# Kernel optimization log

Measured on AMD Instinct MI355X. Metric: run time of the kernel, lower is better.

The kernel has to match this reference:

```python
import jax, jax.numpy as jnp
import numpy as np

C_IN = 128
DIM = 2 * C_IN          # ELAN final channels = 2*in_channels = 256
WS = 8                  # window size
HEADS = 8
HEAD_DIM = DIM // HEADS
B, H, W = 4, 128, 128
LN_EPS = 1e-5


def setup_inputs() -> dict:
    key = jax.random.key(0)
    ks = jax.random.split(key, 20)
    mid = C_IN // 2  # middle_channels == block_channels == 64

    def p(k, shape, scale=0.05):
        return jax.random.normal(k, shape, jnp.float32) * scale

    return dict(
        x=jax.random.normal(ks[0], (B, C_IN, H, W), jnp.float32),
        # ELAN stem 1x1 convs: [main, short], each folded BN (scale, bias)
        w_stem=p(ks[1], (2, mid, C_IN, 1, 1)),
        s_stem=1.0 + p(ks[2], (2, mid)),
        b_stem=p(ks[3], (2, mid)),
        # 2 blocks x 2 convs of 3x3, mid->mid
        w_blk=p(ks[4], (4, mid, mid, 3, 3)),
        s_blk=1.0 + p(ks[5], (4, mid)),
        b_blk=p(ks[6], (4, mid)),
        # SwinV2 block params
        norm1_g=jnp.ones((DIM,), jnp.float32),
        norm1_b=jnp.zeros((DIM,), jnp.float32),
        qkv_w=p(ks[7], (3 * DIM, DIM)),
        qkv_b=p(ks[8], (3 * DIM,)).at[DIM:2 * DIM].set(0.0),  # V2 zeroes k bias
        proj_w=p(ks[9], (DIM, DIM)),
        proj_b=p(ks[10], (DIM,)),
        logit_scale=jnp.full((HEADS, 1, 1), float(np.log(10.0)), jnp.float32),
        cpb_w1=p(ks[11], (512, 2)),
        cpb_b1=p(ks[12], (512,)),
        cpb_w2=p(ks[13], (HEADS, 512)),
        norm2_g=jnp.ones((DIM,), jnp.float32),
        norm2_b=jnp.zeros((DIM,), jnp.float32),
        mlp_w1=p(ks[14], (DIM, DIM)),  # mlp_ratio=1.0
        mlp_b1=p(ks[15], (DIM,)),
        mlp_w2=p(ks[16], (DIM, DIM)),
        mlp_b2=p(ks[17], (DIM,)),
    )


def convbn(x, w, s, b, pad):
    # Conv(no bias) + eval-mode BN folded into per-channel scale/bias + SiLU
    y = jax.lax.conv_general_dilated(
        x, w, (1, 1), [(pad, pad), (pad, pad)],
        dimension_numbers=("NCHW", "OIHW", "NCHW"))
    y = y * s[None, :, None, None] + b[None, :, None, None]
    return jax.nn.silu(y)


def layernorm(x, g, b):
    m = jnp.mean(x, -1, keepdims=True)
    v = jnp.var(x, -1, keepdims=True)
    return (x - m) * jax.lax.rsqrt(v + LN_EPS) * g + b


def _rel_bias_consts():
    ws = WS
    ch = np.arange(-(ws - 1), ws, dtype=np.float32)
    table = np.stack(np.meshgrid(ch, ch, indexing="ij"), axis=-1)  # [2ws-1,2ws-1,2]
    table = table / (ws - 1) * 8.0
    table = np.sign(table) * np.log2(np.abs(table) + 1.0) / 3.0
    coords = np.stack(np.meshgrid(np.arange(ws), np.arange(ws), indexing="ij")).reshape(2, -1)
    rel = (coords[:, :, None] - coords[:, None, :]).transpose(1, 2, 0)  # [N,N,2]
    rel[..., 0] += ws - 1
    rel[..., 1] += ws - 1
    rel[..., 0] *= 2 * ws - 1
    idx = rel.sum(-1).reshape(-1)
    return jnp.asarray(table.reshape(-1, 2)), jnp.asarray(idx)


_TABLE, _IDX = _rel_bias_consts()


def elan_swin(x, w_stem, s_stem, b_stem, w_blk, s_blk, b_blk, norm1_g, norm1_b,
              qkv_w, qkv_b, proj_w, proj_b, logit_scale, cpb_w1, cpb_b1, cpb_w2,
              norm2_g, norm2_b, mlp_w1, mlp_b1, mlp_w2, mlp_b2):
    # ---- ELANBlock ----
    x_short = convbn(x, w_stem[1], s_stem[1], b_stem[1], 0)
    x_main = convbn(x, w_stem[0], s_stem[0], b_stem[0], 0)
    xb = x_main
    outs = []
    for i in range(2):
        xb = convbn(xb, w_blk[2 * i], s_blk[2 * i], b_blk[2 * i], 1)
        xb = convbn(xb, w_blk[2 * i + 1], s_blk[2 * i + 1], b_blk[2 * i + 1], 1)
        outs.append(xb)
    e = jnp.concatenate([outs[1], outs[0], x_main, x_short], axis=1)  # [B,DIM,H,W]
    e = e.transpose(0, 2, 3, 1)  # NHWC

    # ---- ShiftedWindowAttentionV2 (shift=0, H,W divisible by WS) ----
    Bn, Hh, Ww, Cc = e.shape
    nH, nW = Hh // WS, Ww // WS
    N = WS * WS
    xw = e.reshape(Bn, nH, WS, nW, WS, Cc).transpose(0, 1, 3, 2, 4, 5).reshape(-1, N, Cc)
    qkv = xw @ qkv_w.T + qkv_b
    qkv = qkv.reshape(-1, N, 3, HEADS, HEAD_DIM).transpose(2, 0, 3, 1, 4)
    q, k, v = qkv[0], qkv[1], qkv[2]  # [Bw, heads, N, d]
    qn = q / jnp.maximum(jnp.linalg.norm(q, axis=-1, keepdims=True), 1e-12)
    kn = k / jnp.maximum(jnp.linalg.norm(k, axis=-1, keepdims=True), 1e-12)
    attn = jnp.einsum("whnd,whmd->whnm", qn, kn)
    scale = jnp.exp(jnp.minimum(logit_scale, jnp.log(100.0)))  # [heads,1,1]
    attn = attn * scale[None]
    # continuous position bias MLP
    bias = jax.nn.relu(_TABLE @ cpb_w1.T + cpb_b1) @ cpb_w2.T  # [(2ws-1)^2, heads]
    bias = bias[_IDX].reshape(N, N, HEADS).transpose(2, 0, 1)
    bias = 16.0 * jax.nn.sigmoid(bias)
    attn = jax.nn.softmax(attn + bias[None], axis=-1)
    out = jnp.einsum("whnm,whmd->whnd", attn, v).transpose(0, 2, 1, 3).reshape(-1, N, Cc)
    out = out @ proj_w.T + proj_b
    out = out.reshape(Bn, nH, nW, WS, WS, Cc).transpose(0, 1, 3, 2, 4, 5).reshape(Bn, Hh, Ww, Cc)

    # ---- SwinTransformerBlockV2 (post-norm residuals) ----
    s = e + layernorm(out, norm1_g, norm1_b)
    h = s @ mlp_w1.T + mlp_b1
    h = jax.nn.gelu(h, approximate=False)
    h = h @ mlp_w2.T + mlp_b2
    s = s + layernorm(h, norm2_g, norm2_b)
    return s.transpose(0, 3, 1, 2)  # NCHW


def reference(x, w_stem, s_stem, b_stem, w_blk, s_blk, b_blk, norm1_g, norm1_b,
              qkv_w, qkv_b, proj_w, proj_b, logit_scale, cpb_w1, cpb_b1, cpb_w2,
              norm2_g, norm2_b, mlp_w1, mlp_b1, mlp_w2, mlp_b2):
    return elan_swin(x, w_stem, s_stem, b_stem, w_blk, s_blk, b_blk, norm1_g, norm1_b,
                     qkv_w, qkv_b, proj_w, proj_b, logit_scale, cpb_w1, cpb_b1, cpb_w2,
                     norm2_g, norm2_b, mlp_w1, mlp_b1, mlp_w2, mlp_b2)
```

## Files before the change

### kernel.cpp

```cpp
#include <hip/hip_runtime.h>
#include <hip/hip_bf16.h>
#include <math.h>


#define HW 16384
typedef unsigned int u32;
typedef unsigned short u16;
typedef __attribute__((ext_vector_type(8))) short short8;
typedef __attribute__((ext_vector_type(4))) float floatx4;

#define MEMBAR() asm volatile("" ::: "memory")

__device__ __forceinline__ float silu_f(float y) { return y / (1.f + expf(-y)); }
__device__ __forceinline__ float bflo(u32 u) { return __uint_as_float(u << 16); }
__device__ __forceinline__ float bfhi(u32 u) { return __uint_as_float(u & 0xffff0000u); }
__device__ __forceinline__ float bf2f(u16 v) { return __uint_as_float((u32)v << 16); }
__device__ __forceinline__ u16 f2bf(float x) {
  u32 u = __float_as_uint(x);
  u += 0x7fffu + ((u >> 16) & 1u);
  return (u16)(u >> 16);
}
__device__ __forceinline__ u32 pack2(float a, float b) {
  return (u32)f2bf(a) | ((u32)f2bf(b) << 16);
}
__device__ __forceinline__ short8 mk8(u32 a, u32 b, u32 c, u32 d) {
  union { u32 u[4]; short8 s; } t;
  t.u[0] = a; t.u[1] = b; t.u[2] = c; t.u[3] = d;
  return t.s;
}
__device__ __forceinline__ u32 shfl_sel(u32 va, u32 vb, int s, bool sel) {
  u32 x = (u32)__shfl((int)va, s);
  u32 y = (u32)__shfl((int)vb, s);
  return sel ? y : x;
}

#define GLDS16(gp, lp)                                           \
  __builtin_amdgcn_global_load_lds(                              \
      (const __attribute__((address_space(1))) void*)(gp),       \
      (__attribute__((address_space(3))) void*)(lp), 16, 0, 0)

__global__ __launch_bounds__(256) void repack_kernel(
    const float* __restrict__ w_blk, const float* __restrict__ s_blk,
    const float* __restrict__ w_stem, const float* __restrict__ s_stem,
    u16* __restrict__ wtc, u16* __restrict__ wts) {
  int idx = blockIdx.x * 256 + threadIdx.x;
  if (idx < 147456) {
    int c = idx & 63;
    int rest = idx >> 6;
    int oc = rest & 63;
    int ct = rest >> 6;
    int conv = ct / 9, t = ct % 9;
    float w = w_blk[((size_t)(conv * 64 + oc) * 64 + c) * 9 + t];
    wtc[idx] = f2bf(w * s_blk[conv * 64 + oc]);
  } else if (idx < 147456 + 16384) {
    int j = idx - 147456;
    int c = j & 127, oc = j >> 7;
    float w = w_stem[(size_t)oc * 128 + c];
    wts[j] = f2bf(w * s_stem[oc]);
  }
}

__global__ __launch_bounds__(256) void castw_kernel(
    const float* __restrict__ in, u16* __restrict__ outp, int n) {
  int i = blockIdx.x * 256 + threadIdx.x;
  if (i < n) outp[i] = f2bf(in[i]);
}

__global__ __launch_bounds__(512) void cpb_mlp_kernel(
    const float* __restrict__ w1, const float* __restrict__ b1,
    const float* __restrict__ w2, float* __restrict__ pre) {
  __shared__ float hb[512];
  int t = blockIdx.x, j = threadIdx.x;
  int i = t / 15, jj = t % 15;
  float c0 = (float)(i - 7) * (8.f / 7.f);
  float c1 = (float)(jj - 7) * (8.f / 7.f);
  float s0 = (c0 > 0.f) ? 1.f : ((c0 < 0.f) ? -1.f : 0.f);
  float s1 = (c1 > 0.f) ? 1.f : ((c1 < 0.f) ? -1.f : 0.f);
  float t0 = s0 * log2f(fabsf(c0) + 1.f) * (1.f / 3.f);
  float t1 = s1 * log2f(fabsf(c1) + 1.f) * (1.f / 3.f);
  float h = t0 * w1[j * 2] + t1 * w1[j * 2 + 1] + b1[j];
  hb[j] = fmaxf(h, 0.f);
  __syncthreads();
  if (j < 8) {
    float s = 0.f;
    for (int k = 0; k < 512; ++k) s += hb[k] * w2[j * 512 + k];
    pre[t * 8 + j] = s;
  }
}

__global__ __launch_bounds__(256) void cpb_expand_kernel(
    const float* __restrict__ pre, float* __restrict__ bias_t) {
  int idx = blockIdx.x * 256 + threadIdx.x;
  int m = idx >> 6, n = idx & 63;
  int di = (n >> 3) - (m >> 3) + 7;
  int dj = (n & 7) - (m & 7) + 7;
  int ti = di * 15 + dj;
#pragma unroll
  for (int h = 0; h < 8; ++h) {
    float v = pre[ti * 8 + h];
    bias_t[h * 4096 + idx] = 16.f / (1.f + expf(-v));
  }
}

__global__ __launch_bounds__(256) void transpose_in_kernel(
    const float* __restrict__ x, u16* __restrict__ xt) {
  __shared__ float tl[64][65];
  int bid = blockIdx.x;
  int b = bid >> 9;
  int r = bid & 511;
  int cs = r >> 8, hws = r & 255;
  int c0 = cs << 6, hw0 = hws << 6;
  int tid = threadIdx.x;
  for (int e = tid; e < 4096; e += 256) {
    int c = e >> 6, p = e & 63;
    tl[c][p] = x[(size_t)(b * 128 + c0 + c) * HW + hw0 + p];
  }
  __syncthreads();
  for (int e = tid; e < 4096; e += 256) {
    int p = e >> 6, c = e & 63;
    xt[(size_t)(b * HW + hw0 + p) * 128 + c0 + c] = f2bf(tl[c][p]);
  }
}

__global__ __launch_bounds__(256, 4) void gemm_bf16_kernel(
    const u16* __restrict__ A, const u16* __restrict__ W,
    const float* __restrict__ bias, u16* __restrict__ C, int K, int ldc,
    int act) {
  __shared__ u16 As[128 * 64];
  __shared__ u16 Ws[64 * 64];
  int tid = threadIdx.x;
  int wv = tid >> 6, lane = tid & 63;
  int m0 = blockIdx.y * 128, n0 = blockIdx.x * 64;
  floatx4 zz = {0.f, 0.f, 0.f, 0.f};
  floatx4 acc[2][4];
#pragma unroll
  for (int i = 0; i < 2; ++i)
#pragma unroll
    for (int j = 0; j < 4; ++j) acc[i][j] = zz;
  int lr = lane >> 3, ls = lane & 7;
  for (int k0 = 0; k0 < K; k0 += 64) {
#pragma unroll
    for (int i = 0; i < 4; ++i) {
      int ci = wv * 4 + i;
      int r = ci * 8 + lr;
      int cc = ls ^ (r & 7);
      GLDS16(A + (size_t)(m0 + r) * K + k0 + cc * 8, As + ci * 512);
    }
#pragma unroll
    for (int i = 0; i < 2; ++i) {
      int ci = wv * 2 + i;
      int r = ci * 8 + lr;
      int cc = ls ^ (r & 7);
      GLDS16(W + (size_t)(n0 + r) * K + k0 + cc * 8, Ws + ci * 512);
    }
    __syncthreads();
#pragma unroll
    for (int kk = 0; kk < 2; ++kk) {
      int g = kk * 4 + (lane >> 4);
      short8 a0, a1, b0, b1, b2, b3;
      {
        int row = wv * 32 + (lane & 15);
        a0 = *(const short8*)&As[row * 64 + (g ^ (row & 7)) * 8];
        int row2 = row + 16;
        a1 = *(const short8*)&As[row2 * 64 + (g ^ (row2 & 7)) * 8];
      }
      {
        int col = lane & 15;
        b0 = *(const short8*)&Ws[col * 64 + (g ^ (col & 7)) * 8];
        int c1 = col + 16;
        b1 = *(const short8*)&Ws[c1 * 64 + (g ^ (c1 & 7)) * 8];
        int c2 = col + 32;
        b2 = *(const short8*)&Ws[c2 * 64 + (g ^ (c2 & 7)) * 8];
        int c3 = col + 48;
        b3 = *(const short8*)&Ws[c3 * 64 + (g ^ (c3 & 7)) * 8];
      }
      acc[0][0] = __builtin_amdgcn_mfma_f32_16x16x32_bf16(a0, b0, acc[0][0], 0, 0, 0);
      acc[0][1] = __builtin_amdgcn_mfma_f32_16x16x32_bf16(a0, b1, acc[0][1], 0, 0, 0);
      acc[0][2] = __builtin_amdgcn_mfma_f32_16x16x32_bf16(a0, b2, acc[0][2], 0, 0, 0);
      acc[0][3] = __builtin_amdgcn_mfma_f32_16x16x32_bf16(a0, b3, acc[0][3], 0, 0, 0);
      acc[1][0] = __builtin_amdgcn_mfma_f32_16x16x32_bf16(a1, b0, acc[1][0], 0, 0, 0);
      acc[1][1] = __builtin_amdgcn_mfma_f32_16x16x32_bf16(a1, b1, acc[1][1], 0, 0, 0);
      acc[1][2] = __builtin_amdgcn_mfma_f32_16x16x32_bf16(a1, b2, acc[1][2], 0, 0, 0);
      acc[1][3] = __builtin_amdgcn_mfma_f32_16x16x32_bf16(a1, b3, acc[1][3], 0, 0, 0);
    }
    __syncthreads();
  }
  int rbase = wv * 32 + ((lane >> 4) << 2);
  int cb = lane & 15;
#pragma unroll
  for (int mi = 0; mi < 2; ++mi) {
#pragma unroll
    for (int nj = 0; nj < 4; ++nj) {
      int col = n0 + nj * 16 + cb;
      float bv = bias[col];
#pragma unroll
      for (int r = 0; r < 4; ++r) {
        int row = m0 + rbase + mi * 16 + r;
        float v = acc[mi][nj][r] + bv;
        if (act == 1) v = 0.5f * v * (1.f + erff(v * 0.70710678118654752f));
        else if (act == 2) v = silu_f(v);
        C[(size_t)row * ldc + col] = f2bf(v);
      }
    }
  }
}

__global__ __launch_bounds__(256) void conv3x3_mfma_kernel(
    const u16* __restrict__ in, int istr, u16* __restrict__ outp, int ostr,
    const u16* __restrict__ wt, const float* __restrict__ bias) {
  __shared__ u16 tile[6400];
  int tid = threadIdx.x;
  int wv = tid >> 6, lane = tid & 63;
  int bx = blockIdx.x, by = blockIdx.y, b = blockIdx.z;
  int h0 = by * 8, w0 = bx * 8;
#pragma unroll
  for (int rr = 0; rr < 4; ++rr) {
    int slot = rr * 256 + tid;
    int p = slot >> 3, ch = slot & 7;
    if (p < 100) {
      int hr = p / 10, hc = p % 10;
      int gh = h0 + hr - 1, gw = w0 + hc - 1;
      bool ok = (gh >= 0) && (gh < 128) && (gw >= 0) && (gw < 128);
      uint4 v = {0u, 0u, 0u, 0u};
      if (ok) {
        size_t pix = (size_t)((b * 128 + gh) * 128 + gw);
        v = *(const uint4*)(in + pix * istr + ch * 8);
      }
      *(uint4*)(tile + p * 64 + ((ch ^ (p & 7)) << 3)) = v;
    }
  }
  __syncthreads();
  int pl = lane & 15;
  int g = lane >> 4;
  int prow = 2 * wv + (pl >> 3), pcol = pl & 7;
  floatx4 zz = {0.f, 0.f, 0.f, 0.f};
  floatx4 acc[4] = {zz, zz, zz, zz};
#pragma unroll
  for (int t = 0; t < 9; ++t) {
    int dy = t / 3, dx = t % 3;
    int hp = (prow + dy) * 10 + (pcol + dx);
    short8 bf0 = *(const short8*)&tile[hp * 64 + (((0 * 4 + g) ^ (hp & 7)) << 3)];
    short8 bf1 = *(const short8*)&tile[hp * 64 + (((1 * 4 + g) ^ (hp & 7)) << 3)];
    const u16* wtap = wt + t * 4096;
#pragma unroll
    for (int nf = 0; nf < 4; ++nf) {
      short8 a0 = *(const short8*)&wtap[(nf * 16 + pl) * 64 + g * 8];
      short8 a1 = *(const short8*)&wtap[(nf * 16 + pl) * 64 + 32 + g * 8];
      acc[nf] = __builtin_amdgcn_mfma_f32_16x16x32_bf16(a0, bf0, acc[nf], 0, 0, 0);
      acc[nf] = __builtin_amdgcn_mfma_f32_16x16x32_bf16(a1, bf1, acc[nf], 0, 0, 0);
    }
  }
  size_t pix = (size_t)((b * 128 + h0 + prow) * 128 + w0 + pcol);
#pragma unroll
  for (int nf = 0; nf < 4; ++nf) {
    float o0 = silu_f(acc[nf][0] + bias[nf * 16 + g * 4 + 0]);
    float o1 = silu_f(acc[nf][1] + bias[nf * 16 + g * 4 + 1]);
    float o2 = silu_f(acc[nf][2] + bias[nf * 16 + g * 4 + 2]);
    float o3 = silu_f(acc[nf][3] + bias[nf * 16 + g * 4 + 3]);
    uint2 w2;
    w2.x = pack2(o0, o1);
    w2.y = pack2(o2, o3);
    *(uint2*)(outp + pix * ostr + nf * 16 + g * 4) = w2;
  }
}

__device__ __forceinline__ void qkv_mm(const u16* Elds, const u16* qwb,
                                       int moff, int h, int lc, int lg,
                                       floatx4 acc[4][2]) {
  floatx4 zz = {0.f, 0.f, 0.f, 0.f};
#pragma unroll
  for (int mf = 0; mf < 4; ++mf) {
    acc[mf][0] = zz;
    acc[mf][1] = zz;
  }
#pragma unroll
  for (int ks = 0; ks < 8; ++ks) {
    int ch = ks >> 1, g = ((ks & 1) << 2) + lg;
    short8 af[4];
#pragma unroll
    for (int mf = 0; mf < 4; ++mf) {
      int tk = mf * 16 + lc;
      af[mf] = *(const short8*)&Elds[(ch * 64 + tk) * 64 + ((g ^ (tk & 7)) << 3)];
    }
#pragma unroll
    for (int nf = 0; nf < 2; ++nf) {
      short8 bf = *(const short8*)(qwb +
          (size_t)(moff + h * 32 + nf * 16 + lc) * 256 + ks * 32 + lg * 8);
#pragma unroll
      for (int mf = 0; mf < 4; ++mf)
        acc[mf][nf] =
            __builtin_amdgcn_mfma_f32_16x16x32_bf16(af[mf], bf, acc[mf][nf], 0, 0, 0);
    }
  }
}

__global__ __launch_bounds__(512, 4) void attn_fused_kernel(
    const u16* __restrict__ ebf, const u16* __restrict__ qwb,
    const float* __restrict__ qkv_b, const float* __restrict__ logit_scale,
    const float* __restrict__ bias_t, u16* __restrict__ ao) {
  __shared__ __align__(16) char lds[73728];
  int tid = threadIdx.x;
  int w = tid >> 6, l = tid & 63;
  int wid = blockIdx.x;
  int h = __builtin_amdgcn_readfirstlane(w);
  u16* Elds = (u16*)lds;
  char* Sc = lds + 32768 + w * 5120;
  char* Ol = Sc;

  int b = wid >> 8, wh = (wid >> 4) & 15, ww = wid & 15;
  int pixbase = (b << 14) + wh * 1024 + ww * 8;
  {
    int lr = l >> 3, ls = l & 7;
    int ch = w >> 1;
#pragma unroll
    for (int j = 0; j < 4; ++j) {
      int jj = ((w & 1) << 2) + j;
      int pix = pixbase + jj * 128 + lr;
      GLDS16(ebf + (size_t)pix * 256 + ch * 64 + ((ls ^ lr) << 3),
             Elds + (ch * 8 + jj) * 512);
    }
  }
  __syncthreads();

  int lc = l & 15, lg = l >> 4;
  float scale = __expf(fminf(logit_scale[h], 4.6051701860f));
  floatx4 macc[4][2];
  short8 kf[4], qf[4];

  qkv_mm(Elds, qwb, 256, h, lc, lg, macc);
#pragma unroll
  for (int mf = 0; mf < 4; ++mf)
#pragma unroll
    for (int r = 0; r < 4; ++r) {
      float v0 = macc[mf][0][r], v1 = macc[mf][1][r];
      float ss = v0 * v0 + v1 * v1;
      ss += __shfl_xor(ss, 1);
      ss += __shfl_xor(ss, 2);
      ss += __shfl_xor(ss, 4);
      ss += __shfl_xor(ss, 8);
      float rk = 1.f / fmaxf(sqrtf(ss), 1e-12f);
      int tk = mf * 16 + (lg << 2) + r;
      *(u16*)(Sc + tk * 80 + lc * 2) = f2bf(v0 * rk);
      *(u16*)(Sc + tk * 80 + (16 + lc) * 2) = f2bf(v1 * rk);
    }
  MEMBAR();
#pragma unroll
  for (int i = 0; i < 4; ++i)
    kf[i] = *(const short8*)(Sc + (i * 16 + lc) * 80 + (lg << 4));
  MEMBAR();

  qkv_mm(Elds, qwb, 0, h, lc, lg, macc);
  {
    float qb0 = qkv_b[h * 32 + lc], qb1 = qkv_b[h * 32 + 16 + lc];
#pragma unroll
    for (int mf = 0; mf < 4; ++mf)
#pragma unroll
      for (int r = 0; r < 4; ++r) {
        float v0 = macc[mf][0][r] + qb0, v1 = macc[mf][1][r] + qb1;
        float ss = v0 * v0 + v1 * v1;
        ss += __shfl_xor(ss, 1);
        ss += __shfl_xor(ss, 2);
        ss += __shfl_xor(ss, 4);
        ss += __shfl_xor(ss, 8);
        float rq = scale / fmaxf(sqrtf(ss), 1e-12f);
        int tk = mf * 16 + (lg << 2) + r;
        *(u16*)(Sc + tk * 80 + lc * 2) = f2bf(v0 * rq);
        *(u16*)(Sc + tk * 80 + (16 + lc) * 2) = f2bf(v1 * rq);
      }
    MEMBAR();
#pragma unroll
    for (int i = 0; i < 4; ++i)
      qf[i] = *(const short8*)(Sc + (i * 16 + lc) * 80 + (lg << 4));
    MEMBAR();
  }

  u32 v01[4][2], v23[4][2];
  qkv_mm(Elds, qwb, 512, h, lc, lg, macc);
  {
    float vb0 = qkv_b[512 + h * 32 + lc], vb1 = qkv_b[512 + h * 32 + 16 + lc];
#pragma unroll
    for (int mf = 0; mf < 4; ++mf) {
      v01[mf][0] = pack2(macc[mf][0][0] + vb0, macc[mf][0][1] + vb0);
      v23[mf][0] = pack2(macc[mf][0][2] + vb0, macc[mf][0][3] + vb0);
      v01[mf][1] = pack2(macc[mf][1][0] + vb1, macc[mf][1][1] + vb1);
      v23[mf][1] = pack2(macc[mf][1][2] + vb1, macc[mf][1][3] + vb1);
    }
  }

  floatx4 zz = {0.f, 0.f, 0.f, 0.f};
  floatx4 S[4][4];
#pragma unroll
  for (int mi = 0; mi < 4; ++mi)
#pragma unroll
    for (int ni = 0; ni < 4; ++ni)
      S[mi][ni] = __builtin_amdgcn_mfma_f32_16x16x32_bf16(kf[mi], qf[ni], zz, 0, 0, 0);

  const float* bh = bias_t + h * 4096;
  float den[4] = {0.f, 0.f, 0.f, 0.f};
#pragma unroll
  for (int mi = 0; mi < 4; ++mi) {
    int mb = mi * 16 + (lg << 2);
#pragma unroll
    for (int ni = 0; ni < 4; ++ni) {
      int nn = ni * 16 + lc;
#pragma unroll
      for (int r = 0; r < 4; ++r) {
        float e = __expf(S[mi][ni][r] + bh[(mb + r) * 64 + nn]);
        S[mi][ni][r] = e;
        den[ni] += e;
      }
    }
  }
#pragma unroll
  for (int ni = 0; ni < 4; ++ni) {
    den[ni] += __shfl_xor(den[ni], 16);
    den[ni] += __shfl_xor(den[ni], 32);
    den[ni] = 1.f / den[ni];
  }
  u32 p01[4][4], p23[4][4];
#pragma unroll
  for (int mi = 0; mi < 4; ++mi)
#pragma unroll
    for (int ni = 0; ni < 4; ++ni) {
      p01[mi][ni] = pack2(S[mi][ni][0] * den[ni], S[mi][ni][1] * den[ni]);
      p23[mi][ni] = pack2(S[mi][ni][2] * den[ni], S[mi][ni][3] * den[ni]);
    }

  int s1 = ((lg & 1) << 5) + lc;
  int s2 = s1 + 16;
  bool hi = lg >= 2;
  short8 vf[2][2];
#pragma unroll
  for (int ks = 0; ks < 2; ++ks)
#pragma unroll
    for (int db = 0; db < 2; ++db) {
      u32 w0 = shfl_sel(v01[ks * 2][db], v01[ks * 2 + 1][db], s1, hi);
      u32 w1 = shfl_sel(v23[ks * 2][db], v23[ks * 2 + 1][db], s1, hi);
      u32 w2 = shfl_sel(v01[ks * 2][db], v01[ks * 2 + 1][db], s2, hi);
      u32 w3 = shfl_sel(v23[ks * 2][db], v23[ks * 2 + 1][db], s2, hi);
      vf[ks][db] = mk8(w0, w1, w2, w3);
    }
  floatx4 O[4][2];
#pragma unroll
  for (int nb = 0; nb < 4; ++nb) {
    u32 a0 = shfl_sel(p01[0][nb], p01[1][nb], s1, hi);
    u32 a1 = shfl_sel(p23[0][nb], p23[1][nb], s1, hi);
    u32 a2 = shfl_sel(p01[0][nb], p01[1][nb], s2, hi);
    u32 a3 = shfl_sel(p23[0][nb], p23[1][nb], s2, hi);
    short8 pf0 = mk8(a0, a1, a2, a3);
    u32 b0 = shfl_sel(p01[2][nb], p01[3][nb], s1, hi);
    u32 b1 = shfl_sel(p23[2][nb], p23[3][nb], s1, hi);
    u32 b2 = shfl_sel(p01[2][nb], p01[3][nb], s2, hi);
    u32 b3 = shfl_sel(p23[2][nb], p23[3][nb], s2, hi);
    short8 pf1 = mk8(b0, b1, b2, b3);
    floatx4 o0 = __builtin_amdgcn_mfma_f32_16x16x32_bf16(pf0, vf[0][0], zz, 0, 0, 0);
    o0 = __builtin_amdgcn_mfma_f32_16x16x32_bf16(pf1, vf[1][0], o0, 0, 0, 0);
    floatx4 o1 = __builtin_amdgcn_mfma_f32_16x16x32_bf16(pf0, vf[0][1], zz, 0, 0, 0);
    o1 = __builtin_amdgcn_mfma_f32_16x16x32_bf16(pf1, vf[1][1], o1, 0, 0, 0);
    O[nb][0] = o0;
    O[nb][1] = o1;
  }

#pragma unroll
  for (int nb = 0; nb < 4; ++nb)
#pragma unroll
    for (int r = 0; r < 4; ++r) {
      int n = nb * 16 + (lg << 2) + r;
      *(u16*)(Ol + n * 72 + lc * 2) = f2bf(O[nb][0][r]);
      *(u16*)(Ol + n * 72 + (16 + lc) * 2) = f2bf(O[nb][1][r]);
    }
  MEMBAR();
  u32 ov[16];
#pragma unroll
  for (int j = 0; j < 16; ++j) ov[j] = *(const u32*)(Ol + l * 72 + j * 4);
  uint4* op = (uint4*)(ao + (size_t)(wid * 64 + l) * 256 + h * 32);
#pragma unroll
  for (int q4 = 0; q4 < 4; ++q4) {
    uint4 v;
    v.x = ov[q4 * 4 + 0];
    v.y = ov[q4 * 4 + 1];
    v.z = ov[q4 * 4 + 2];
    v.w = ov[q4 * 4 + 3];
    op[q4] = v;
  }
}

__global__ __launch_bounds__(256) void ln1v_kernel(
    const u16* __restrict__ pin, const u16* __restrict__ ebf,
    u16* __restrict__ sbf, const float* __restrict__ g,
    const float* __restrict__ bb) {
  int tid = threadIdx.x;
  int bid = blockIdx.x;
  int b = bid >> 8, hw0 = (bid & 255) << 6;
  int i = tid >> 2, qq = tid & 3;
  int hw = hw0 + i;
  int him = hw >> 7, wim = hw & 127;
  int wid = b * 256 + (him >> 3) * 16 + (wim >> 3);
  int t = wid * 64 + (him & 7) * 8 + (wim & 7);
  size_t pbase = (size_t)t * 256 + qq * 64;
  size_t ebase = ((size_t)(b * HW + hw)) * 256 + qq * 64;
  float v[64];
  float s1 = 0.f, s2 = 0.f;
#pragma unroll
  for (int j = 0; j < 8; ++j) {
    uint4 u = *(const uint4*)(pin + pbase + j * 8);
    u32 ua[4] = {u.x, u.y, u.z, u.w};
#pragma unroll
    for (int k = 0; k < 4; ++k) {
      float a = bflo(ua[k]), c = bfhi(ua[k]);
      v[j * 8 + 2 * k] = a;
      v[j * 8 + 2 * k + 1] = c;
      s1 += a + c;
      s2 += a * a + c * c;
    }
  }
  s1 += __shfl_xor(s1, 1);
  s1 += __shfl_xor(s1, 2);
  s2 += __shfl_xor(s2, 1);
  s2 += __shfl_xor(s2, 2);
  float mean = s1 * (1.f / 256.f);
  float var = s2 * (1.f / 256.f) - mean * mean;
  float rs = rsqrtf(var + 1e-5f);
#pragma unroll
  for (int j = 0; j < 8; ++j) {
    uint4 u = *(const uint4*)(ebf + ebase + j * 8);
    u32 ua[4] = {u.x, u.y, u.z, u.w};
    uint4 o;
    u32 ow[4];
#pragma unroll
    for (int k = 0; k < 4; ++k) {
      int c = qq * 64 + j * 8 + 2 * k;
      float o0 = bflo(ua[k]) + (v[j * 8 + 2 * k] - mean) * rs * g[c] + bb[c];
      float o1 = bfhi(ua[k]) + (v[j * 8 + 2 * k + 1] - mean) * rs * g[c + 1] + bb[c + 1];
      ow[k] = pack2(o0, o1);
    }
    o.x = ow[0]; o.y = ow[1]; o.z = ow[2]; o.w = ow[3];
    *(uint4*)(sbf + ebase + j * 8) = o;
  }
}

__global__ __launch_bounds__(256) void ln2t_kernel(
    const u16* __restrict__ h2, const u16* __restrict__ sbf,
    const float* __restrict__ g, const float* __restrict__ bb,
    float* __restrict__ outp) {
  __shared__ float tile[64][257];
  int tid = threadIdx.x;
  int bid = blockIdx.x;
  int b = bid >> 8, hw0 = (bid & 255) << 6;
  int i = tid >> 2, qq = tid & 3;
  size_t base = ((size_t)(b * HW + hw0 + i)) * 256 + qq * 64;
  float v[64];
  float s1 = 0.f, s2 = 0.f;
#pragma unroll
  for (int j = 0; j < 8; ++j) {
    uint4 u = *(const uint4*)(h2 + base + j * 8);
    u32 ua[4] = {u.x, u.y, u.z, u.w};
#pragma unroll
    for (int k = 0; k < 4; ++k) {
      float a = bflo(ua[k]), c = bfhi(ua[k]);
      v[j * 8 + 2 * k] = a;
      v[j * 8 + 2 * k + 1] = c;
      s1 += a + c;
      s2 += a * a + c * c;
    }
  }
  s1 += __shfl_xor(s1, 1);
  s1 += __shfl_xor(s1, 2);
  s2 += __shfl_xor(s2, 1);
  s2 += __shfl_xor(s2, 2);
  float mean = s1 * (1.f / 256.f);
  float var = s2 * (1.f / 256.f) - mean * mean;
  float rs = rsqrtf(var + 1e-5f);
#pragma unroll
  for (int j = 0; j < 8; ++j) {
    uint4 u = *(const uint4*)(sbf + base + j * 8);
    u32 ua[4] = {u.x, u.y, u.z, u.w};
#pragma unroll
    for (int k = 0; k < 4; ++k) {
      int c = qq * 64 + j * 8 + 2 * k;
      tile[i][c] = bflo(ua[k]) + (v[j * 8 + 2 * k] - mean) * rs * g[c] + bb[c];
      tile[i][c + 1] = bfhi(ua[k]) + (v[j * 8 + 2 * k + 1] - mean) * rs * g[c + 1] + bb[c + 1];
    }
  }
  __syncthreads();
  int pl = tid & 63, cq = tid >> 6;
#pragma unroll 8
  for (int cc = 0; cc < 64; ++cc) {
    int c = cq * 64 + cc;
    outp[((size_t)(b * 256 + c)) * HW + hw0 + pl] = tile[pl][c];
  }
}

extern "C" void kernel_launch(void* const* d_in, const int* in_sizes, int n_in,
                              void* d_out, int out_size, void* d_ws, size_t ws_size,
                              hipStream_t stream) {
  const float* x        = (const float*)d_in[0];
  const float* w_stem   = (const float*)d_in[1];
  const float* s_stem   = (const float*)d_in[2];
  const float* b_stem   = (const float*)d_in[3];
  const float* w_blk    = (const float*)d_in[4];
  const float* s_blk    = (const float*)d_in[5];
  const float* b_blk    = (const float*)d_in[6];
  const float* norm1_g  = (const float*)d_in[7];
  const float* norm1_b  = (const float*)d_in[8];
  const float* qkv_w    = (const float*)d_in[9];
  const float* qkv_b    = (const float*)d_in[10];
  const float* proj_w   = (const float*)d_in[11];
  const float* proj_b   = (const float*)d_in[12];
  const float* logit_sc = (const float*)d_in[13];
  const float* cpb_w1   = (const float*)d_in[14];
  const float* cpb_b1   = (const float*)d_in[15];
  const float* cpb_w2   = (const float*)d_in[16];
  const float* norm2_g  = (const float*)d_in[17];
  const float* norm2_b  = (const float*)d_in[18];
  const float* mlp_w1   = (const float*)d_in[19];
  const float* mlp_b1   = (const float*)d_in[20];
  const float* mlp_w2   = (const float*)d_in[21];
  const float* mlp_b2   = (const float*)d_in[22];
  float* out = (float*)d_out;
  float* ws = (float*)d_ws;
  (void)in_sizes; (void)n_in; (void)out_size; (void)ws_size;

  float* R0 = ws;
  float* R1 = ws + 16777216;
  float* R2 = ws + 33554432;
  float* TAIL = ws + 50331648;
  u16* WTC  = (u16*)TAIL;
  u16* WTS  = (u16*)(TAIL + 73728);
  u16* QWB  = (u16*)(TAIL + 81920);
  u16* PWB  = (u16*)(TAIL + 180224);
  u16* M1WB = (u16*)(TAIL + 212992);
  u16* M2WB = (u16*)(TAIL + 245760);
  float* BPRE = TAIL + 278528;
  float* BFT  = TAIL + 280576;

  u16* XT  = (u16*)R2;
  u16* EBF = (u16*)(R2 + 8388608);
  u16* T1  = (u16*)R1;
  u16* T2  = (u16*)(R1 + 2097152);
  u16* AO  = (u16*)R0;
  u16* P   = (u16*)(R0 + 8388608);
  u16* SBF = (u16*)R0;
  u16* Hb  = (u16*)R2;
  u16* H2  = (u16*)(R0 + 8388608);

  repack_kernel<<<640, 256, 0, stream>>>(w_blk, s_blk, w_stem, s_stem, WTC, WTS);
  castw_kernel<<<768, 256, 0, stream>>>(qkv_w, QWB, 196608);
  castw_kernel<<<256, 256, 0, stream>>>(proj_w, PWB, 65536);
  castw_kernel<<<256, 256, 0, stream>>>(mlp_w1, M1WB, 65536);
  castw_kernel<<<256, 256, 0, stream>>>(mlp_w2, M2WB, 65536);
  cpb_mlp_kernel<<<225, 512, 0, stream>>>(cpb_w1, cpb_b1, cpb_w2, BPRE);
  cpb_expand_kernel<<<16, 256, 0, stream>>>(BPRE, BFT);

  transpose_in_kernel<<<2048, 256, 0, stream>>>(x, XT);
  dim3 gs(2, 512);
  gemm_bf16_kernel<<<gs, 256, 0, stream>>>(XT, WTS, b_stem, EBF + 128, 128, 256, 2);

  dim3 cgrid(16, 16, 4);
  conv3x3_mfma_kernel<<<cgrid, 256, 0, stream>>>(EBF + 128, 256, T1, 64, WTC, b_blk);
  conv3x3_mfma_kernel<<<cgrid, 256, 0, stream>>>(T1, 64, EBF + 64, 256, WTC + 9 * 4096, b_blk + 64);
  conv3x3_mfma_kernel<<<cgrid, 256, 0, stream>>>(EBF + 64, 256, T2, 64, WTC + 18 * 4096, b_blk + 128);
  conv3x3_mfma_kernel<<<cgrid, 256, 0, stream>>>(T2, 64, EBF, 256, WTC + 27 * 4096, b_blk + 192);

  attn_fused_kernel<<<1024, 512, 0, stream>>>(EBF, QWB, qkv_b, logit_sc, BFT, AO);

  dim3 g4(4, 512);
  gemm_bf16_kernel<<<g4, 256, 0, stream>>>(AO, PWB, proj_b, P, 256, 256, 0);
  ln1v_kernel<<<1024, 256, 0, stream>>>(P, EBF, SBF, norm1_g, norm1_b);
  gemm_bf16_kernel<<<g4, 256, 0, stream>>>(SBF, M1WB, mlp_b1, Hb, 256, 256, 1);
  gemm_bf16_kernel<<<g4, 256, 0, stream>>>(Hb, M2WB, mlp_b2, H2, 256, 256, 0);
  ln2t_kernel<<<1024, 256, 0, stream>>>(H2, SBF, norm2_g, norm2_b, out);
}
```

Measured before the change: 421.3 us.

## Fuse MLP second GEMM with LayerNorm2 and merge weight-cast kernels

Replaces the final mlp_w2 GEMM plus separate ln2t kernel with one kernel that computes a full 64x256 output tile, stages it in LDS, applies LayerNorm and the residual, and writes NCHW output directly. This removes the H2 intermediate round trip through global memory and one launch. It also merges the repack and four weight-cast kernels into a single prep kernel to cut launch overhead. The trade-off is that the fused kernel writes the output with strided per-element stores across channels instead of the old LDS-transposed coalesced stores, and it keeps 16 accumulators per wave.

```diff
diff --git a/kernel.cpp b/kernel.cpp
--- a/kernel.cpp
+++ b/kernel.cpp
@@ -39,10 +39,13 @@
       (const __attribute__((address_space(1))) void*)(gp),       \
       (__attribute__((address_space(3))) void*)(lp), 16, 0, 0)
 
-__global__ __launch_bounds__(256) void repack_kernel(
+__global__ __launch_bounds__(256) void prep_kernel(
     const float* __restrict__ w_blk, const float* __restrict__ s_blk,
     const float* __restrict__ w_stem, const float* __restrict__ s_stem,
-    u16* __restrict__ wtc, u16* __restrict__ wts) {
+    const float* __restrict__ qkv_w, const float* __restrict__ proj_w,
+    const float* __restrict__ mlp_w1, const float* __restrict__ mlp_w2,
+    u16* __restrict__ wtc, u16* __restrict__ wts, u16* __restrict__ qwb,
+    u16* __restrict__ pwb, u16* __restrict__ m1wb, u16* __restrict__ m2wb) {
   int idx = blockIdx.x * 256 + threadIdx.x;
   if (idx < 147456) {
     int c = idx & 63;
@@ -52,18 +55,23 @@
     int conv = ct / 9, t = ct % 9;
     float w = w_blk[((size_t)(conv * 64 + oc) * 64 + c) * 9 + t];
     wtc[idx] = f2bf(w * s_blk[conv * 64 + oc]);
-  } else if (idx < 147456 + 16384) {
+  } else if (idx < 163840) {
     int j = idx - 147456;
     int c = j & 127, oc = j >> 7;
-    float w = w_stem[(size_t)oc * 128 + c];
-    wts[j] = f2bf(w * s_stem[oc]);
-  }
-}
-
-__global__ __launch_bounds__(256) void castw_kernel(
-    const float* __restrict__ in, u16* __restrict__ outp, int n) {
-  int i = blockIdx.x * 256 + threadIdx.x;
-  if (i < n) outp[i] = f2bf(in[i]);
+    wts[j] = f2bf(w_stem[(size_t)oc * 128 + c] * s_stem[oc]);
+  } else if (idx < 360448) {
+    int j = idx - 163840;
+    qwb[j] = f2bf(qkv_w[j]);
+  } else if (idx < 425984) {
+    int j = idx - 360448;
+    pwb[j] = f2bf(proj_w[j]);
+  } else if (idx < 491520) {
+    int j = idx - 425984;
+    m1wb[j] = f2bf(mlp_w1[j]);
+  } else if (idx < 557056) {
+    int j = idx - 491520;
+    m2wb[j] = f2bf(mlp_w2[j]);
+  }
 }
 
 __global__ __launch_bounds__(512) void cpb_mlp_kernel(
@@ -539,27 +547,70 @@
   }
 }
 
-__global__ __launch_bounds__(256) void ln2t_kernel(
-    const u16* __restrict__ h2, const u16* __restrict__ sbf,
-    const float* __restrict__ g, const float* __restrict__ bb,
-    float* __restrict__ outp) {
-  __shared__ float tile[64][257];
+__global__ __launch_bounds__(256, 4) void gemm_ln2_kernel(
+    const u16* __restrict__ A, const u16* __restrict__ W,
+    const float* __restrict__ bias, const float* __restrict__ g,
+    const float* __restrict__ bb, const u16* __restrict__ res,
+    float* __restrict__ outf) {
+  __shared__ __align__(16) char lds[40960];
+  u16* As = (u16*)lds;
+  u16* Ws = (u16*)(lds + 8192);
+  u16* Ct = (u16*)lds;
   int tid = threadIdx.x;
-  int bid = blockIdx.x;
-  int b = bid >> 8, hw0 = (bid & 255) << 6;
+  int w = tid >> 6, l = tid & 63;
+  int lr = l >> 3, ls = l & 7;
+  int lc = l & 15, lg = l >> 4;
+  int m0 = blockIdx.x << 6;
+  floatx4 zz = {0.f, 0.f, 0.f, 0.f};
+  floatx4 acc[16];
+#pragma unroll
+  for (int i = 0; i < 16; ++i) acc[i] = zz;
+  for (int k0 = 0; k0 < 256; k0 += 64) {
+#pragma unroll
+    for (int j = 0; j < 2; ++j) {
+      int ci = w * 2 + j;
+      int r = ci * 8 + lr;
+      GLDS16(A + (size_t)(m0 + r) * 256 + k0 + ((ls ^ (r & 7)) << 3),
+             As + ci * 512);
+    }
+#pragma unroll
+    for (int j = 0; j < 8; ++j) {
+      int ci = w * 8 + j;
+      int r = ci * 8 + lr;
+      GLDS16(W + (size_t)r * 256 + k0 + ((ls ^ (r & 7)) << 3), Ws + ci * 512);
+    }
+    __syncthreads();
+#pragma unroll
+    for (int kk = 0; kk < 2; ++kk) {
+      int gg = (kk << 2) + lg;
+      int arow = w * 16 + lc;
+      short8 af = *(const short8*)&As[arow * 64 + ((gg ^ (arow & 7)) << 3)];
+#pragma unroll
+      for (int nf = 0; nf < 16; ++nf) {
+        int crow = nf * 16 + lc;
+        short8 bf = *(const short8*)&Ws[crow * 64 + ((gg ^ (crow & 7)) << 3)];
+        acc[nf] = __builtin_amdgcn_mfma_f32_16x16x32_bf16(af, bf, acc[nf], 0, 0, 0);
+      }
+    }
+    __syncthreads();
+  }
+#pragma unroll
+  for (int nf = 0; nf < 16; ++nf) {
+    float bv = bias[nf * 16 + lc];
+#pragma unroll
+    for (int r = 0; r < 4; ++r)
+      Ct[(w * 16 + (lg << 2) + r) * 264 + nf * 16 + lc] = f2bf(acc[nf][r] + bv);
+  }
+  __syncthreads();
   int i = tid >> 2, qq = tid & 3;
-  size_t base = ((size_t)(b * HW + hw0 + i)) * 256 + qq * 64;
-  float v[64];
   float s1 = 0.f, s2 = 0.f;
 #pragma unroll
-  for (int j = 0; j < 8; ++j) {
-    uint4 u = *(const uint4*)(h2 + base + j * 8);
+  for (int j2 = 0; j2 < 8; ++j2) {
+    uint4 u = *(const uint4*)&Ct[i * 264 + qq * 64 + j2 * 8];
     u32 ua[4] = {u.x, u.y, u.z, u.w};
 #pragma unroll
     for (int k = 0; k < 4; ++k) {
       float a = bflo(ua[k]), c = bfhi(ua[k]);
-      v[j * 8 + 2 * k] = a;
-      v[j * 8 + 2 * k + 1] = c;
       s1 += a + c;
       s2 += a * a + c * c;
     }
@@ -571,23 +622,23 @@
   float mean = s1 * (1.f / 256.f);
   float var = s2 * (1.f / 256.f) - mean * mean;
   float rs = rsqrtf(var + 1e-5f);
-#pragma unroll
-  for (int j = 0; j < 8; ++j) {
-    uint4 u = *(const uint4*)(sbf + base + j * 8);
+  int p = m0 + i;
+  int b = p >> 14, hw = p & 16383;
+  size_t rbase = (size_t)p * 256 + qq * 64;
+#pragma unroll
+  for (int j2 = 0; j2 < 8; ++j2) {
+    uint4 cu = *(const uint4*)&Ct[i * 264 + qq * 64 + j2 * 8];
+    u32 ca[4] = {cu.x, cu.y, cu.z, cu.w};
+    uint4 u = *(const uint4*)(res + rbase + j2 * 8);
     u32 ua[4] = {u.x, u.y, u.z, u.w};
 #pragma unroll
     for (int k = 0; k < 4; ++k) {
-      int c = qq * 64 + j * 8 + 2 * k;
-      tile[i][c] = bflo(ua[k]) + (v[j * 8 + 2 * k] - mean) * rs * g[c] + bb[c];
-      tile[i][c + 1] = bfhi(ua[k]) + (v[j * 8 + 2 * k + 1] - mean) * rs * g[c + 1] + bb[c + 1];
-    }
-  }
-  __syncthreads();
-  int pl = tid & 63, cq = tid >> 6;
-#pragma unroll 8
-  for (int cc = 0; cc < 64; ++cc) {
-    int c = cq * 64 + cc;
-    outp[((size_t)(b * 256 + c)) * HW + hw0 + pl] = tile[pl][c];
+      int c = qq * 64 + j2 * 8 + 2 * k;
+      float o0 = bflo(ua[k]) + (bflo(ca[k]) - mean) * rs * g[c] + bb[c];
+      float o1 = bfhi(ua[k]) + (bfhi(ca[k]) - mean) * rs * g[c + 1] + bb[c + 1];
+      outf[(size_t)(b * 256 + c) * HW + hw] = o0;
+      outf[(size_t)(b * 256 + c + 1) * HW + hw] = o1;
+    }
   }
 }
 
@@ -642,13 +693,10 @@
   u16* P   = (u16*)(R0 + 8388608);
   u16* SBF = (u16*)R0;
   u16* Hb  = (u16*)R2;
-  u16* H2  = (u16*)(R0 + 8388608);
-
-  repack_kernel<<<640, 256, 0, stream>>>(w_blk, s_blk, w_stem, s_stem, WTC, WTS);
-  castw_kernel<<<768, 256, 0, stream>>>(qkv_w, QWB, 196608);
-  castw_kernel<<<256, 256, 0, stream>>>(proj_w, PWB, 65536);
-  castw_kernel<<<256, 256, 0, stream>>>(mlp_w1, M1WB, 65536);
-  castw_kernel<<<256, 256, 0, stream>>>(mlp_w2, M2WB, 65536);
+
+  prep_kernel<<<2176, 256, 0, stream>>>(w_blk, s_blk, w_stem, s_stem, qkv_w,
+                                        proj_w, mlp_w1, mlp_w2, WTC, WTS, QWB,
+                                        PWB, M1WB, M2WB);
   cpb_mlp_kernel<<<225, 512, 0, stream>>>(cpb_w1, cpb_b1, cpb_w2, BPRE);
   cpb_expand_kernel<<<16, 256, 0, stream>>>(BPRE, BFT);
 
@@ -668,6 +716,6 @@
   gemm_bf16_kernel<<<g4, 256, 0, stream>>>(AO, PWB, proj_b, P, 256, 256, 0);
   ln1v_kernel<<<1024, 256, 0, stream>>>(P, EBF, SBF, norm1_g, norm1_b);
   gemm_bf16_kernel<<<g4, 256, 0, stream>>>(SBF, M1WB, mlp_b1, Hb, 256, 256, 1);
-  gemm_bf16_kernel<<<g4, 256, 0, stream>>>(Hb, M2WB, mlp_b2, H2, 256, 256, 0);
-  ln2t_kernel<<<1024, 256, 0, stream>>>(H2, SBF, norm2_g, norm2_b, out);
-}
+  gemm_ln2_kernel<<<1024, 256, 0, stream>>>(Hb, M2WB, mlp_b2, norm2_g, norm2_b,
+                                            SBF, out);
+}
```

Measured after the change: 410.1 us (median of 3 runs). 2.7% less time.
